# Performance work log

Measured on AMD Instinct MI355X. Metric: run time of the kernel, lower is better.

Reference implementation:

```python
import jax, jax.numpy as jnp
import numpy as np

D_IN = 768
D_SAE = 768 * 16  # expansion_factor = 16
K = 64
BATCH = 8192


def setup_inputs() -> dict:
    key = jax.random.key(0)
    k1, k2, k3 = jax.random.split(key, 3)
    x = jax.random.normal(k1, (BATCH, D_IN), dtype=jnp.float32)
    # Kaiming-uniform-ish encoder init (exact init values don't matter for correctness)
    bound = (6.0 / D_IN) ** 0.5
    W_enc = jax.random.uniform(k2, (D_IN, D_SAE), dtype=jnp.float32, minval=-bound, maxval=bound)
    b_enc = jnp.zeros((D_SAE,), dtype=jnp.float32)
    W_dec = jax.random.normal(k3, (D_SAE, D_IN), dtype=jnp.float32) * (1.0 / D_IN ** 0.5)
    # unit-norm decoder rows (per the module's normalize_decoder_weights)
    W_dec = W_dec / (jnp.linalg.norm(W_dec, axis=1, keepdims=True) + 1e-8)
    b_dec = jnp.zeros((D_IN,), dtype=jnp.float32)
    return {"x": x, "W_enc": W_enc, "b_enc": b_enc, "W_dec": W_dec, "b_dec": b_dec}


def reference(x, W_enc, b_enc, W_dec, b_dec):
    # encode: center, dense matmul, ReLU
    pre_acts = jax.nn.relu((x - b_dec) @ W_enc + b_enc)  # [B, d_sae]
    # top-k selection per row, scatter back into dense sparse_acts
    topk_vals, topk_idx = jax.lax.top_k(pre_acts, K)  # [B, K]
    rows = jnp.arange(pre_acts.shape[0])[:, None]  # [B, 1]
    sparse_acts = jnp.zeros_like(pre_acts).at[rows, topk_idx].set(topk_vals)
    # decode: dense matmul + bias
    reconstruction = sparse_acts @ W_dec + b_dec  # [B, d_in]
    return (reconstruction, sparse_acts)
```

## Files before the change

### kernel.cpp

```cpp
#include <hip/hip_runtime.h>
#include <hip/hip_fp16.h>
#include <stdint.h>

#define D_IN   768
#define D_SAE  12288
#define BATCH  8192
#define K_TOP  64
#define CAND_MAX 256

typedef _Float16 f16;
typedef _Float16 v8h __attribute__((ext_vector_type(8)));
typedef float v4f __attribute__((ext_vector_type(4)));

__device__ inline void async16(const void* g, void* l) {
    __builtin_amdgcn_global_load_lds(
        (const __attribute__((address_space(1))) unsigned int*)g,
        (__attribute__((address_space(3))) unsigned int*)l, 16, 0, 0);
}

__global__ __launch_bounds__(256) void k_convert_x(
    const float* __restrict__ x, const float* __restrict__ b_dec,
    f16* __restrict__ xhi)
{
    int i4 = (blockIdx.x * 256 + threadIdx.x) * 4;
    float4 v = *(const float4*)(x + i4);
    int col = i4 % D_IN;
    float vv[4] = { v.x - b_dec[col], v.y - b_dec[col + 1],
                    v.z - b_dec[col + 2], v.w - b_dec[col + 3] };
    union { short4 s; f16 h[4]; } H;
#pragma unroll
    for (int u = 0; u < 4; ++u) H.h[u] = (f16)vv[u];
    *(short4*)(xhi + i4) = H.s;
}

__global__ __launch_bounds__(256) void k_convert_wt(
    const float* __restrict__ W, f16* __restrict__ whiT, f16* __restrict__ wloT)
{
    __shared__ float tile[32][33];
    const int n0 = blockIdx.x * 32;
    const int k0 = blockIdx.y * 32;
    const int c = threadIdx.x & 31;
    const int rr = threadIdx.x >> 5;
#pragma unroll
    for (int s = 0; s < 4; ++s) {
        int r = s * 8 + rr;
        tile[r][c] = W[(size_t)(k0 + r) * D_SAE + n0 + c];
    }
    __syncthreads();
#pragma unroll
    for (int s = 0; s < 4; ++s) {
        int r2 = s * 8 + rr;
        float v = tile[c][r2];
        f16 hi = (f16)v;
        f16 lo = (f16)(v - (float)hi);
        whiT[(size_t)(n0 + r2) * D_IN + k0 + c] = hi;
        wloT[(size_t)(n0 + r2) * D_IN + k0 + c] = lo;
    }
}

__global__ __launch_bounds__(256) void k_convert_wd(
    const float* __restrict__ W, f16* __restrict__ Wh)
{
    int i4 = (blockIdx.x * 256 + threadIdx.x) * 4;
    float4 v = *(const float4*)(W + i4);
    union { short4 s; f16 h[4]; } H;
    H.h[0] = (f16)v.x; H.h[1] = (f16)v.y; H.h[2] = (f16)v.z; H.h[3] = (f16)v.w;
    *(short4*)(Wh + i4) = H.s;
}

__global__ __launch_bounds__(256) void k_gemm_f16(
    const f16* __restrict__ A,
    const f16* __restrict__ Bt,
    const float* __restrict__ b_enc,
    f16* __restrict__ outap)
{
    __shared__ f16 Asm[2][128 * 32];
    __shared__ f16 Bsm[2][128 * 32];
    const int tid  = threadIdx.x;
    const int wave = tid >> 6;
    const int lane = tid & 63;
    const int bn = blockIdx.x * 128;
    const int bm = blockIdx.y * 128;

    const int r16  = lane >> 2;
    const int kc8  = (lane & 3) * 8;
    const int mrow = lane & 15;
    const int quad = lane >> 4;
    const int wm = (wave & 1) * 64;
    const int wn = (wave >> 1) * 64;

    v4f acc[4][4] = {};

    const f16* gA = A  + (size_t)(bm + wave * 32 + r16) * D_IN + kc8;
    const f16* gB = Bt + (size_t)(bn + wave * 32 + r16) * D_IN + kc8;
    f16* lA[2] = { &Asm[0][(wave * 32) * 32], &Asm[1][(wave * 32) * 32] };
    f16* lB[2] = { &Bsm[0][(wave * 32) * 32], &Bsm[1][(wave * 32) * 32] };

    #define STAGE(b, kk)                                   \
        do {                                               \
            async16(gA + (kk),            lA[b]);          \
            async16(gA + (kk) + 16*D_IN,  lA[b] + 16*32);  \
            async16(gB + (kk),            lB[b]);          \
            async16(gB + (kk) + 16*D_IN,  lB[b] + 16*32);  \
        } while (0)

    STAGE(0, 0);
#pragma unroll 2
    for (int it = 0; it < 24; ++it) {
        const int cur = it & 1;
        __syncthreads();
        if (it + 1 < 24) STAGE(cur ^ 1, (it + 1) * 32);
        v8h af[4], bf[4];
#pragma unroll
        for (int i = 0; i < 4; ++i)
            af[i] = *(const v8h*)&Asm[cur][(wm + i * 16 + mrow) * 32 + quad * 8];
#pragma unroll
        for (int j = 0; j < 4; ++j)
            bf[j] = *(const v8h*)&Bsm[cur][(wn + j * 16 + mrow) * 32 + quad * 8];
#pragma unroll
        for (int i = 0; i < 4; ++i)
#pragma unroll
            for (int j = 0; j < 4; ++j)
                acc[i][j] = __builtin_amdgcn_mfma_f32_16x16x32_f16(af[i], bf[j], acc[i][j], 0, 0, 0);
    }
    #undef STAGE

#pragma unroll
    for (int i = 0; i < 4; ++i) {
#pragma unroll
        for (int r = 0; r < 4; ++r) {
            int grow = bm + wm + i * 16 + quad * 4 + r;
            f16* op = outap + (size_t)grow * (2 * D_SAE) + bn + wn;
#pragma unroll
            for (int j = 0; j < 4; ++j) {
                int c = j * 16 + mrow;
                float val = acc[i][j][r] + b_enc[bn + wn + c];
                __builtin_nontemporal_store((f16)(val > 0.f ? val : 0.f), op + c);
            }
        }
    }
}

__device__ __forceinline__ unsigned suffix_scan_256(unsigned h, int t, unsigned* wtot, unsigned* tot_out) {
    const int lane = t & 63;
    const int w = t >> 6;
    unsigned s = h;
#pragma unroll
    for (int off = 1; off < 64; off <<= 1) {
        unsigned o = __shfl_down(s, off);
        if (lane + off < 64) s += o;
    }
    if (lane == 0) wtot[w] = s;
    __syncthreads();
    unsigned suf = s;
    unsigned tot = 0;
#pragma unroll
    for (int w2 = 0; w2 < 4; ++w2) {
        tot += wtot[w2];
        if (w2 > w) suf += wtot[w2];
    }
    *tot_out = tot;
    return suf;
}

__global__ __launch_bounds__(256) void k_topk2(
    float* __restrict__ sparse,
    const float* __restrict__ x,
    const f16* __restrict__ WhiT, const f16* __restrict__ WloT,
    const float* __restrict__ b_enc,
    const f16* __restrict__ Wdh,
    const float* __restrict__ b_dec,
    float* __restrict__ recon)
{
    const int row = blockIdx.x;
    const int t = threadIdx.x;
    const int lane = t & 63;
    float* rp = sparse + (size_t)row * D_SAE;
    const f16* ap = (const f16*)rp;

    v8h av[6];
#pragma unroll
    for (int j = 0; j < 6; ++j)
        av[j] = __builtin_nontemporal_load((const v8h*)(ap + ((size_t)j * 256 + t) * 8));

    __shared__ unsigned hist[256];
    __shared__ unsigned wtot[4];
    __shared__ float sh_cutoff;
    __shared__ int sh_ncand;
    __shared__ int   cand_i[CAND_MAX];
    __shared__ float cand_v[CAND_MAX];
    __shared__ float kept_v[K_TOP];
    __shared__ int   kept_i[K_TOP];
    __shared__ float xr[D_IN];

    const float margin = 0.05f;

    hist[t] = 0;
    if (t == 0) sh_ncand = 0;
    for (int k = t; k < D_IN; k += 256)
        xr[k] = x[(size_t)row * D_IN + k] - b_dec[k];
    __syncthreads();

#pragma unroll
    for (int j = 0; j < 6; ++j)
#pragma unroll
        for (int u = 0; u < 8; ++u) {
            float x0 = (float)av[j][u];
            if (x0 >= 2.0f) {
                int b = (int)((x0 - 2.0f) * 32.0f); if (b > 255) b = 255;
                atomicAdd(&hist[b], 1u);
            }
        }
    __syncthreads();
    unsigned h0 = hist[t];
    unsigned tot0;
    unsigned suf0 = suffix_scan_256(h0, t, wtot, &tot0);
    if (tot0 >= K_TOP) {
        if (suf0 >= K_TOP && suf0 - h0 < K_TOP)
            sh_cutoff = fmaxf(2.0f + (float)t * (1.0f / 32.0f) - margin, 1e-30f);
    }
    __syncthreads();
    if (tot0 < K_TOP) {
        hist[t] = 0;
        __syncthreads();
#pragma unroll
        for (int j = 0; j < 6; ++j)
#pragma unroll
            for (int u = 0; u < 8; ++u) {
                float x0 = (float)av[j][u];
                if (x0 >= 0.25f) {
                    int b = (int)(x0 * 32.0f); if (b > 255) b = 255;
                    atomicAdd(&hist[b], 1u);
                }
            }
        __syncthreads();
        unsigned h1 = hist[t];
        unsigned tot1;
        unsigned suf1 = suffix_scan_256(h1, t, wtot, &tot1);
        if (tot1 >= K_TOP) {
            if (suf1 >= K_TOP && suf1 - h1 < K_TOP)
                sh_cutoff = fmaxf((float)t * (1.0f / 32.0f) - margin, 1e-30f);
        }
        __syncthreads();
        if (tot1 < K_TOP) {
            hist[t] = 0;
            __syncthreads();
#pragma unroll
            for (int j = 0; j < 6; ++j)
#pragma unroll
                for (int u = 0; u < 8; ++u) {
                    float x0 = (float)av[j][u];
                    if (x0 > 0.0f && x0 < 0.25f) {
                        int b = (int)(x0 * 1024.0f); if (b > 255) b = 255;
                        atomicAdd(&hist[b], 1u);
                    }
                }
            __syncthreads();
            unsigned h2 = hist[t];
            unsigned tot2;
            unsigned suf2 = suffix_scan_256(h2, t, wtot, &tot2);
            unsigned need = K_TOP - tot1;
            if (tot2 >= need) {
                if (suf2 >= need && suf2 - h2 < need)
                    sh_cutoff = fmaxf((float)t * (1.0f / 1024.0f) - margin, 1e-30f);
            } else {
                if (t == 0) sh_cutoff = 1e-30f;
            }
        }
    }
    __syncthreads();
    const float cutoff = sh_cutoff;

#pragma unroll
    for (int j = 0; j < 6; ++j)
#pragma unroll
        for (int u = 0; u < 8; ++u) {
            float x0 = (float)av[j][u];
            bool pass = (x0 >= cutoff);
            unsigned long long m = __ballot(pass);
            if (m != 0ull) {
                int leader = (int)__builtin_ctzll(m);
                int cnt = (int)__builtin_popcountll(m);
                int base0 = 0;
                if (lane == leader) base0 = atomicAdd(&sh_ncand, cnt);
                base0 = __shfl(base0, leader);
                if (pass) {
                    int pos = base0 + (int)__builtin_popcountll(m & ((1ull << lane) - 1ull));
                    if (pos < CAND_MAX) { cand_i[pos] = (j * 256 + t) * 8 + u; cand_v[pos] = x0; }
                }
            }
        }
    __syncthreads();
    int ncand = sh_ncand; if (ncand > CAND_MAX) ncand = CAND_MAX;

    for (int c = t; c < ncand; c += 256) {
        const f16* wh = WhiT + (size_t)cand_i[c] * D_IN;
        const f16* wl = WloT + (size_t)cand_i[c] * D_IN;
        float acc = 0.f;
        for (int k = 0; k < D_IN; k += 8) {
            v8h hv = *(const v8h*)(wh + k);
            v8h lv = *(const v8h*)(wl + k);
#pragma unroll
            for (int u = 0; u < 8; ++u)
                acc += xr[k + u] * ((float)hv[u] + (float)lv[u]);
        }
        acc += b_enc[cand_i[c]];
        cand_v[c] = acc > 0.f ? acc : 0.f;
    }
    __syncthreads();

    for (int c = t; c < ncand; c += 256) {
        float vc = cand_v[c]; int ic = cand_i[c];
        int r = 0;
        for (int m = 0; m < ncand; ++m) {
            float vm = cand_v[m];
            r += (vm > vc || (vm == vc && cand_i[m] < ic)) ? 1 : 0;
        }
        if (r < K_TOP) { kept_v[r] = vc; kept_i[r] = ic; }
    }
    __syncthreads();
    int nk = ncand < K_TOP ? ncand : K_TOP;

#pragma unroll
    for (int j = 0; j < 12; ++j) {
        v4f z = {0.f, 0.f, 0.f, 0.f};
        __builtin_nontemporal_store(z, (v4f*)(rp + ((size_t)j * 256 + t) * 4));
    }
    __syncthreads();
    if (t < nk) rp[kept_i[t]] = kept_v[t];

    float r0 = b_dec[t], r1 = b_dec[t + 256], r2 = b_dec[t + 512];
#pragma unroll 4
    for (int m = 0; m < nk; ++m) {
        float val = kept_v[m];
        const f16* wr = Wdh + (size_t)kept_i[m] * D_IN;
        r0 += val * (float)wr[t];
        r1 += val * (float)wr[t + 256];
        r2 += val * (float)wr[t + 512];
    }
    float* rc = recon + (size_t)row * D_IN;
    __builtin_nontemporal_store(r0, rc + t);
    __builtin_nontemporal_store(r1, rc + t + 256);
    __builtin_nontemporal_store(r2, rc + t + 512);
}

extern "C" void kernel_launch(void* const* d_in, const int* in_sizes, int n_in,
                              void* d_out, int out_size, void* d_ws, size_t ws_size,
                              hipStream_t stream) {
    const float* x     = (const float*)d_in[0];
    const float* W_enc = (const float*)d_in[1];
    const float* b_enc = (const float*)d_in[2];
    const float* W_dec = (const float*)d_in[3];
    const float* b_dec = (const float*)d_in[4];
    float* out    = (float*)d_out;
    float* recon  = out;
    float* sparse = out + (size_t)BATCH * D_IN;

    const size_t xplane = (size_t)BATCH * D_IN;
    const size_t wplane = (size_t)D_SAE * D_IN;
    f16* xhi  = (f16*)d_ws;
    f16* whiT = xhi + xplane;
    f16* wloT = whiT + wplane;
    f16* wdh  = wloT + wplane;

    k_convert_x<<<xplane / 1024, 256, 0, stream>>>(x, b_dec, xhi);
    k_convert_wt<<<dim3(D_SAE / 32, D_IN / 32), 256, 0, stream>>>(W_enc, whiT, wloT);
    k_convert_wd<<<wplane / 1024, 256, 0, stream>>>(W_dec, wdh);
    k_gemm_f16<<<dim3(D_SAE / 128, BATCH / 128), 256, 0, stream>>>(xhi, whiT, b_enc, (f16*)sparse);
    k_topk2<<<BATCH, 256, 0, stream>>>(sparse, x, whiT, wloT, b_enc, wdh, b_dec, recon);
}
```

Measured before the change: 1.210 ms.

## Load both K halves per step in GEMM and move half of sparse zeroing into GEMM

The GEMM main loop drops the double-buffered prefetch. Each iteration now loads two 32-wide K slices into both LDS buffers, synchronises, and runs MFMAs on both, which halves the number of barrier rounds but no longer overlaps loads with compute. The upper half of each sparse output row, beyond the f16 staging region, is now zeroed at the end of the GEMM kernel, so the top-k kernel only zeroes the first half. The zeroing moves into a compute-bound kernel, but it depends on the top-k kernel reading the f16 staging data before overwriting it, and it changes the ordering assumptions.

```diff
diff --git a/kernel.cpp b/kernel.cpp
--- a/kernel.cpp
+++ b/kernel.cpp
@@ -93,37 +93,43 @@
 
     const f16* gA = A  + (size_t)(bm + wave * 32 + r16) * D_IN + kc8;
     const f16* gB = Bt + (size_t)(bn + wave * 32 + r16) * D_IN + kc8;
-    f16* lA[2] = { &Asm[0][(wave * 32) * 32], &Asm[1][(wave * 32) * 32] };
-    f16* lB[2] = { &Bsm[0][(wave * 32) * 32], &Bsm[1][(wave * 32) * 32] };
-
-    #define STAGE(b, kk)                                   \
-        do {                                               \
-            async16(gA + (kk),            lA[b]);          \
-            async16(gA + (kk) + 16*D_IN,  lA[b] + 16*32);  \
-            async16(gB + (kk),            lB[b]);          \
-            async16(gB + (kk) + 16*D_IN,  lB[b] + 16*32);  \
-        } while (0)
-
-    STAGE(0, 0);
-#pragma unroll 2
-    for (int it = 0; it < 24; ++it) {
-        const int cur = it & 1;
-        __syncthreads();
-        if (it + 1 < 24) STAGE(cur ^ 1, (it + 1) * 32);
-        v8h af[4], bf[4];
-#pragma unroll
-        for (int i = 0; i < 4; ++i)
-            af[i] = *(const v8h*)&Asm[cur][(wm + i * 16 + mrow) * 32 + quad * 8];
-#pragma unroll
-        for (int j = 0; j < 4; ++j)
-            bf[j] = *(const v8h*)&Bsm[cur][(wn + j * 16 + mrow) * 32 + quad * 8];
-#pragma unroll
-        for (int i = 0; i < 4; ++i)
+    f16* lA0  = &Asm[0][(wave * 32) * 32];
+    f16* lA0b = &Asm[0][(wave * 32 + 16) * 32];
+    f16* lB0  = &Bsm[0][(wave * 32) * 32];
+    f16* lB0b = &Bsm[0][(wave * 32 + 16) * 32];
+    f16* lA1  = &Asm[1][(wave * 32) * 32];
+    f16* lA1b = &Asm[1][(wave * 32 + 16) * 32];
+    f16* lB1  = &Bsm[1][(wave * 32) * 32];
+    f16* lB1b = &Bsm[1][(wave * 32 + 16) * 32];
+
+    for (int k0 = 0; k0 < D_IN; k0 += 64) {
+        __syncthreads();
+        async16(gA + k0,               lA0);
+        async16(gA + k0 + 16 * D_IN,   lA0b);
+        async16(gB + k0,               lB0);
+        async16(gB + k0 + 16 * D_IN,   lB0b);
+        async16(gA + k0 + 32,              lA1);
+        async16(gA + k0 + 32 + 16 * D_IN,  lA1b);
+        async16(gB + k0 + 32,              lB1);
+        async16(gB + k0 + 32 + 16 * D_IN,  lB1b);
+        __syncthreads();
+
+#pragma unroll
+        for (int s = 0; s < 2; ++s) {
+            v8h af[4], bf[4];
+#pragma unroll
+            for (int i = 0; i < 4; ++i)
+                af[i] = *(const v8h*)&Asm[s][(wm + i * 16 + mrow) * 32 + quad * 8];
 #pragma unroll
             for (int j = 0; j < 4; ++j)
-                acc[i][j] = __builtin_amdgcn_mfma_f32_16x16x32_f16(af[i], bf[j], acc[i][j], 0, 0, 0);
-    }
-    #undef STAGE
+                bf[j] = *(const v8h*)&Bsm[s][(wn + j * 16 + mrow) * 32 + quad * 8];
+#pragma unroll
+            for (int i = 0; i < 4; ++i)
+#pragma unroll
+                for (int j = 0; j < 4; ++j)
+                    acc[i][j] = __builtin_amdgcn_mfma_f32_16x16x32_f16(af[i], bf[j], acc[i][j], 0, 0, 0);
+        }
+    }
 
 #pragma unroll
     for (int i = 0; i < 4; ++i) {
@@ -138,6 +144,18 @@
                 __builtin_nontemporal_store((f16)(val > 0.f ? val : 0.f), op + c);
             }
         }
+    }
+
+    {
+        float* zbase = (float*)outap;
+        const int r = tid >> 1;
+        const int half = (tid & 1) * 32;
+        float* zp = zbase + (size_t)(bm + r) * D_SAE + (D_SAE / 2)
+                  + blockIdx.x * 64 + half;
+        v4f z = {0.f, 0.f, 0.f, 0.f};
+#pragma unroll
+        for (int q = 0; q < 8; ++q)
+            __builtin_nontemporal_store(z, (v4f*)(zp + q * 4));
     }
 }
 
@@ -322,7 +340,7 @@
     int nk = ncand < K_TOP ? ncand : K_TOP;
 
 #pragma unroll
-    for (int j = 0; j < 12; ++j) {
+    for (int j = 0; j < 6; ++j) {
         v4f z = {0.f, 0.f, 0.f, 0.f};
         __builtin_nontemporal_store(z, (v4f*)(rp + ((size_t)j * 256 + t) * 4));
     }
@@ -358,10 +376,10 @@
 
     const size_t xplane = (size_t)BATCH * D_IN;
     const size_t wplane = (size_t)D_SAE * D_IN;
-    f16* xhi  = (f16*)d_ws;
-    f16* whiT = xhi + xplane;
-    f16* wloT = whiT + wplane;
-    f16* wdh  = wloT + wplane;
+    f16* xhi    = (f16*)d_ws;
+    f16* whiT   = xhi + xplane;
+    f16* wloT   = whiT + wplane;
+    f16* wdh    = wloT + wplane;
 
     k_convert_x<<<xplane / 1024, 256, 0, stream>>>(x, b_dec, xhi);
     k_convert_wt<<<dim3(D_SAE / 32, D_IN / 32), 256, 0, stream>>>(W_enc, whiT, wloT);
```

New measurement: 1.362 ms. +12.5%, slower.
